# Kernel tuning notes

Measured on AMD Instinct MI355X. Metric: run time of the kernel, lower is better.

The kernel has to match this reference:

```python
import jax, jax.numpy as jnp
import numpy as np

D = 64        # state dim (num_output)
H = 256       # MLP hidden width
B = 4096      # batch
NUM_STEPS = 16  # fixed-step Dormand-Prince steps over t in [0,1] per bijector


def _mlp(t, y, W1, b1, W2, b2, W3, b3):
    # time-conditioned MLP: concat scalar t to state, two tanh layers, linear out
    tcol = jnp.full((y.shape[0], 1), t, dtype=y.dtype)
    h = jnp.tanh(jnp.concatenate([y, tcol], axis=1) @ W1 + b1)
    h = jnp.tanh(h @ W2 + b2)
    return h @ W3 + b3


def _dopri5_fixed(f, y0):
    # classic Dormand-Prince (RK45) Butcher tableau, 5th-order solution,
    # fixed step h = 1/NUM_STEPS from t=0 to t=1
    h = jnp.asarray(1.0 / NUM_STEPS, dtype=y0.dtype)

    def step(y, i):
        t = i.astype(y0.dtype) * h
        k1 = f(t, y)
        k2 = f(t + h * (1/5),  y + h * ((1/5) * k1))
        k3 = f(t + h * (3/10), y + h * ((3/40) * k1 + (9/40) * k2))
        k4 = f(t + h * (4/5),  y + h * ((44/45) * k1 - (56/15) * k2 + (32/9) * k3))
        k5 = f(t + h * (8/9),  y + h * ((19372/6561) * k1 - (25360/2187) * k2
                                        + (64448/6561) * k3 - (212/729) * k4))
        k6 = f(t + h,          y + h * ((9017/3168) * k1 - (355/33) * k2
                                        + (46732/5247) * k3 + (49/176) * k4
                                        - (5103/18656) * k5))
        y_next = y + h * ((35/384) * k1 + (500/1113) * k3 + (125/192) * k4
                          - (2187/6784) * k5 + (11/84) * k6)
        return y_next, None

    y_final, _ = jax.lax.scan(step, y0, jnp.arange(NUM_STEPS))
    return y_final


def setup_inputs() -> dict:
    key = jax.random.key(0)
    ks = jax.random.split(key, 7)
    s_in = 1.0 / np.sqrt(D + 1)
    s_h = 1.0 / np.sqrt(H)
    inp = {"x": jax.random.normal(ks[0], (B, D), dtype=jnp.float32)}
    for i, base in enumerate([1, 4]):
        inp[f"p{i}_W1"] = jax.random.normal(ks[base], (D + 1, H), dtype=jnp.float32) * s_in
        inp[f"p{i}_b1"] = jnp.zeros((H,), dtype=jnp.float32)
        inp[f"p{i}_W2"] = jax.random.normal(ks[base + 1], (H, H), dtype=jnp.float32) * s_h
        inp[f"p{i}_b2"] = jnp.zeros((H,), dtype=jnp.float32)
        inp[f"p{i}_W3"] = jax.random.normal(ks[base + 2], (H, D), dtype=jnp.float32) * s_h
        inp[f"p{i}_b3"] = jnp.zeros((D,), dtype=jnp.float32)
    return inp


def reference(x, p0_W1, p0_b1, p0_W2, p0_b2, p0_W3, p0_b3,
              p1_W1, p1_b1, p1_W2, p1_b2, p1_W3, p1_b3):
    # Chain(list(reversed(bijectors))).forward applies bijector 0 first, then 1.
    # FFJORD bijector forward = integrate dz/dt = mlp(t, z) from t=0 to t=1.
    y = x
    params = [(p0_W1, p0_b1, p0_W2, p0_b2, p0_W3, p0_b3),
              (p1_W1, p1_b1, p1_W2, p1_b2, p1_W3, p1_b3)]
    for (W1, b1, W2, b2, W3, b3) in params:
        f = lambda t, z: _mlp(t, z, W1, b1, W2, b2, W3, b3)
        y = _dopri5_fixed(f, y)
    return y
```

## Files before the change

kernel.cpp:

```cpp
#include <hip/hip_runtime.h>

typedef __attribute__((ext_vector_type(8))) short short8;
typedef __attribute__((ext_vector_type(4))) float f32x4;

#define NSTEPS 16

__device__ __forceinline__ unsigned short bf16rne(float f) {
  unsigned int u = __float_as_uint(f);
  u += 0x7FFFu + ((u >> 16) & 1u);
  return (unsigned short)(u >> 16);
}

#if __has_builtin(__builtin_amdgcn_cvt_pk_bf16_f32)
typedef __attribute__((ext_vector_type(2))) __bf16 v2bf16;
__device__ __forceinline__ unsigned int pk2(float a, float b) {
  v2bf16 t = __builtin_amdgcn_cvt_pk_bf16_f32(a, b);
  unsigned int r;
  __builtin_memcpy(&r, &t, 4);
  return r;
}
#else
__device__ __forceinline__ unsigned int pk2(float a, float b) {
  unsigned int ua = __float_as_uint(a), ub = __float_as_uint(b);
  ua += 0x7FFFu + ((ua >> 16) & 1u);
  ub += 0x7FFFu + ((ub >> 16) & 1u);
  return (ua >> 16) | (ub & 0xFFFF0000u);
}
#endif

__device__ __forceinline__ float tanh_fast(float x) {
  float e = __builtin_amdgcn_exp2f(x * 2.8853900817779268f);
  return __builtin_fmaf(-2.0f, __builtin_amdgcn_rcpf(e + 1.0f), 1.0f);
}

__global__ void ffjord_setup(const float* __restrict__ W1a, const float* __restrict__ W2a,
                             const float* __restrict__ W3a, const float* __restrict__ W1b,
                             const float* __restrict__ W2b, const float* __restrict__ W3b,
                             unsigned short* __restrict__ ws) {
  int gid = blockIdx.x * blockDim.x + threadIdx.x;
  int bij = gid / 12288;
  int r = gid - bij * 12288;
  const float* W1 = bij ? W1b : W1a;
  const float* W2 = bij ? W2b : W2a;
  const float* W3 = bij ? W3b : W3a;
  unsigned short* o = ws + bij * 98304;
  const float* src;
  int kstride;
  if (r < 2048) {
    int lane = r & 63, nt = (r >> 6) & 15, ks = r >> 10;
    int k0 = ks * 32 + (lane >> 4) * 8, n = nt * 16 + (lane & 15);
    src = W1 + k0 * 256 + n; kstride = 256; o += r * 8;
  } else if (r < 10240) {
    int rr = r - 2048;
    int lane = rr & 63, nt = (rr >> 6) & 15, ks = rr >> 10;
    int k0 = ks * 32 + (lane >> 4) * 8, n = nt * 16 + (lane & 15);
    src = W2 + k0 * 256 + n; kstride = 256; o += 16384 + rr * 8;
  } else {
    int rr = r - 10240;
    int lane = rr & 63, nt = (rr >> 6) & 3, ks = rr >> 8;
    int k0 = ks * 32 + (lane >> 4) * 8, n = nt * 16 + (lane & 15);
    src = W3 + k0 * 64 + n; kstride = 64; o += 81920 + rr * 8;
  }
  #pragma unroll
  for (int j = 0; j < 8; j++) o[j] = bf16rne(src[j * kstride]);
}

__global__ __launch_bounds__(512, 2) void ffjord_main(
    const float* __restrict__ x, float* __restrict__ out,
    const unsigned short* __restrict__ ws,
    const float* __restrict__ W1a, const float* __restrict__ b1a,
    const float* __restrict__ b2a, const float* __restrict__ b3a,
    const float* __restrict__ W1b, const float* __restrict__ b1b,
    const float* __restrict__ b2b, const float* __restrict__ b3b) {
  __shared__ __align__(16) unsigned short zA[1088];
  __shared__ __align__(16) unsigned short h1A[4096];
  __shared__ __align__(16) unsigned short h2A[4096];
  __shared__ __align__(16) float fbuf[2][16 * 68];

  const int tid = threadIdx.x;
  const int wave = tid >> 6;
  const int lane = tid & 63;
  const int cl = lane & 15;
  const int qd = lane >> 4;
  const int kh = wave >> 2;
  const int mt3 = wave & 3;
  const int c3 = mt3 * 16 + qd * 4;
  const int row0 = blockIdx.x * 16;
  const int row = tid >> 5;
  const int d0 = (tid & 31) * 2;

  const int zoff = ((d0 >> 5) * 4 + ((d0 >> 3) & 3)) * 136 + row * 8 + (d0 & 7);
  const int zrb = qd * 136 + cl * 8;

  int hoff[2];
  #pragma unroll
  for (int t = 0; t < 2; t++) {
    int c0 = (wave * 2 + t) * 16 + qd * 4;
    hoff[t] = (c0 >> 5) * 512 + ((c0 & 31) >> 3) * 128 + cl * 8 + (c0 & 7);
  }

  const float hstep = 1.0f / 16.0f;

  float y[2];
  {
    float2 v = *(const float2*)(x + (row0 + row) * 64 + d0);
    y[0] = v.x; y[1] = v.y;
  }
  float k[6][2];

  const float ACO[6][5] = {
      {0.f, 0.f, 0.f, 0.f, 0.f},
      {1.f / 5.f, 0.f, 0.f, 0.f, 0.f},
      {3.f / 40.f, 9.f / 40.f, 0.f, 0.f, 0.f},
      {44.f / 45.f, -56.f / 15.f, 32.f / 9.f, 0.f, 0.f},
      {19372.f / 6561.f, -25360.f / 2187.f, 64448.f / 6561.f, -212.f / 729.f, 0.f},
      {9017.f / 3168.f, -355.f / 33.f, 46732.f / 5247.f, 49.f / 176.f, -5103.f / 18656.f}};
  const float CT[6] = {0.0f, 0.2f, 0.3f, 0.8f, 8.0f / 9.0f, 1.0f};
  const float BW0 = 35.f / 384.f, BW2 = 500.f / 1113.f, BW3 = 125.f / 192.f,
              BW4 = -2187.f / 6784.f, BW5 = 11.f / 84.f;

  for (int bij = 0; bij < 2; bij++) {
    const unsigned short* wsb = ws + bij * 98304;
    const float* W1 = bij ? W1b : W1a;
    const float* b1 = bij ? b1b : b1a;
    const float* b2 = bij ? b2b : b2a;
    const float* b3 = bij ? b3b : b3a;

    f32x4 b1c[2], w1t4[2], b2c[2];
    #pragma unroll
    for (int t = 0; t < 2; t++) {
      int c0 = (wave * 2 + t) * 16 + qd * 4;
      b1c[t] = *(const f32x4*)(b1 + c0);
      w1t4[t] = *(const f32x4*)(W1 + 64 * 256 + c0);
      b2c[t] = *(const f32x4*)(b2 + c0);
    }
    f32x4 b3c;
    if (kh == 0) b3c = *(const f32x4*)(b3 + c3);
    else { b3c[0] = 0.f; b3c[1] = 0.f; b3c[2] = 0.f; b3c[3] = 0.f; }

    const short8* w1p = (const short8*)wsb;
    const short8* w2p = (const short8*)(wsb + 16384);
    const short8* w3p = (const short8*)(wsb + 81920);
    short8 w1f[2][2];
    #pragma unroll
    for (int ks = 0; ks < 2; ks++)
      #pragma unroll
      for (int t = 0; t < 2; t++)
        w1f[ks][t] = w1p[(ks * 16 + wave * 2 + t) * 64 + lane];
    short8 w2f[8][2];
    #pragma unroll
    for (int ks = 0; ks < 8; ks++)
      #pragma unroll
      for (int t = 0; t < 2; t++)
        w2f[ks][t] = w2p[(ks * 16 + wave * 2 + t) * 64 + lane];
    short8 w3f[4];
    #pragma unroll
    for (int kk = 0; kk < 4; kk++)
      w3f[kk] = w3p[((kh * 4 + kk) * 4 + mt3) * 64 + lane];

    for (int step = 0; step < NSTEPS; step++) {
      float stepf = (float)step;
      #pragma unroll
      for (int s = 0; s < 6; s++) {
        float ts = (stepf + CT[s]) * hstep;

        {
          float z0 = y[0], z1 = y[1];
          #pragma unroll
          for (int j = 0; j < 5; j++)
            if (j < s) {
              float a = hstep * ACO[s][j];
              z0 += a * k[j][0];
              z1 += a * k[j][1];
            }
          *(unsigned int*)(zA + zoff) = pk2(z0, z1);
        }
        __syncthreads();

        {
          short8 a0 = *(const short8*)(zA + zrb);
          short8 a1 = *(const short8*)(zA + zrb + 544);
          #pragma unroll
          for (int t = 0; t < 2; t++) {
            f32x4 acc;
            #pragma unroll
            for (int r = 0; r < 4; r++)
              acc[r] = __builtin_fmaf(ts, w1t4[t][r], b1c[t][r]);
            acc = __builtin_amdgcn_mfma_f32_16x16x32_bf16(w1f[0][t], a0, acc, 0, 0, 0);
            acc = __builtin_amdgcn_mfma_f32_16x16x32_bf16(w1f[1][t], a1, acc, 0, 0, 0);
            uint2 pv;
            pv.x = pk2(tanh_fast(acc[0]), tanh_fast(acc[1]));
            pv.y = pk2(tanh_fast(acc[2]), tanh_fast(acc[3]));
            *(uint2*)(h1A + hoff[t]) = pv;
          }
        }
        __syncthreads();

        {
          f32x4 accA[2], accB[2];
          #pragma unroll
          for (int t = 0; t < 2; t++) {
            accA[t] = b2c[t];
            accB[t][0] = 0.f; accB[t][1] = 0.f; accB[t][2] = 0.f; accB[t][3] = 0.f;
          }
          #pragma unroll
          for (int ks = 0; ks < 4; ks++) {
            short8 hb = ((const short8*)h1A)[ks * 64 + lane];
            accA[0] = __builtin_amdgcn_mfma_f32_16x16x32_bf16(w2f[ks][0], hb, accA[0], 0, 0, 0);
            accA[1] = __builtin_amdgcn_mfma_f32_16x16x32_bf16(w2f[ks][1], hb, accA[1], 0, 0, 0);
          }
          #pragma unroll
          for (int ks = 4; ks < 8; ks++) {
            short8 hb = ((const short8*)h1A)[ks * 64 + lane];
            accB[0] = __builtin_amdgcn_mfma_f32_16x16x32_bf16(w2f[ks][0], hb, accB[0], 0, 0, 0);
            accB[1] = __builtin_amdgcn_mfma_f32_16x16x32_bf16(w2f[ks][1], hb, accB[1], 0, 0, 0);
          }
          #pragma unroll
          for (int t = 0; t < 2; t++) {
            uint2 pv;
            pv.x = pk2(tanh_fast(accA[t][0] + accB[t][0]), tanh_fast(accA[t][1] + accB[t][1]));
            pv.y = pk2(tanh_fast(accA[t][2] + accB[t][2]), tanh_fast(accA[t][3] + accB[t][3]));
            *(uint2*)(h2A + hoff[t]) = pv;
          }
        }
        __syncthreads();

        {
          f32x4 accP = b3c;
          f32x4 accQ; accQ[0] = 0.f; accQ[1] = 0.f; accQ[2] = 0.f; accQ[3] = 0.f;
          short8 hb0 = ((const short8*)h2A)[(kh * 4 + 0) * 64 + lane];
          short8 hb1 = ((const short8*)h2A)[(kh * 4 + 1) * 64 + lane];
          short8 hb2 = ((const short8*)h2A)[(kh * 4 + 2) * 64 + lane];
          short8 hb3 = ((const short8*)h2A)[(kh * 4 + 3) * 64 + lane];
          accP = __builtin_amdgcn_mfma_f32_16x16x32_bf16(w3f[0], hb0, accP, 0, 0, 0);
          accP = __builtin_amdgcn_mfma_f32_16x16x32_bf16(w3f[1], hb1, accP, 0, 0, 0);
          accQ = __builtin_amdgcn_mfma_f32_16x16x32_bf16(w3f[2], hb2, accQ, 0, 0, 0);
          accQ = __builtin_amdgcn_mfma_f32_16x16x32_bf16(w3f[3], hb3, accQ, 0, 0, 0);
          f32x4 res;
          #pragma unroll
          for (int r = 0; r < 4; r++) res[r] = accP[r] + accQ[r];
          *(f32x4*)(&fbuf[kh][cl * 68 + c3]) = res;
        }
        __syncthreads();

        {
          float2 fa = *(const float2*)(&fbuf[0][row * 68 + d0]);
          float2 fb = *(const float2*)(&fbuf[1][row * 68 + d0]);
          k[s][0] = fa.x + fb.x;
          k[s][1] = fa.y + fb.y;
        }
      }

      #pragma unroll
      for (int i = 0; i < 2; i++) {
        float d = BW0 * k[0][i] + BW2 * k[2][i] + BW3 * k[3][i] +
                  BW4 * k[4][i] + BW5 * k[5][i];
        y[i] += hstep * d;
      }
    }
  }

  float2 o2; o2.x = y[0]; o2.y = y[1];
  *(float2*)(out + (row0 + row) * 64 + d0) = o2;
}

extern "C" void kernel_launch(void* const* d_in, const int* in_sizes, int n_in,
                              void* d_out, int out_size, void* d_ws, size_t ws_size,
                              hipStream_t stream) {
  (void)in_sizes; (void)n_in; (void)out_size; (void)ws_size;
  const float* x   = (const float*)d_in[0];
  const float* W1a = (const float*)d_in[1];
  const float* b1a = (const float*)d_in[2];
  const float* W2a = (const float*)d_in[3];
  const float* b2a = (const float*)d_in[4];
  const float* W3a = (const float*)d_in[5];
  const float* b3a = (const float*)d_in[6];
  const float* W1b = (const float*)d_in[7];
  const float* b1b = (const float*)d_in[8];
  const float* W2b = (const float*)d_in[9];
  const float* b2b = (const float*)d_in[10];
  const float* W3b = (const float*)d_in[11];
  const float* b3b = (const float*)d_in[12];
  unsigned short* ws = (unsigned short*)d_ws;
  float* out = (float*)d_out;

  hipLaunchKernelGGL(ffjord_setup, dim3(96), dim3(256), 0, stream,
                     W1a, W2a, W3a, W1b, W2b, W3b, ws);
  hipLaunchKernelGGL(ffjord_main, dim3(256), dim3(512), 0, stream,
                     x, out, ws, W1a, b1a, b2a, b3a, W1b, b1b, b2b, b3b);
}
```

Measured before the change: 332.2 us.

## Double block to 1024 threads, one 16-column tile per wave

Each block now runs 16 waves instead of 8. Every wave owns a single 16-column tile of the hidden layers instead of two, the final layer's K dimension is split four ways across waves, and each thread tracks one state element instead of two. The aim is more parallel waves per 16-row tile to hide MFMA and barrier latency in this serial RK chain, with lower register pressure per thread. In exchange there is a wider block-level __syncthreads, a four-way fbuf reduction, narrower per-thread stores, and weight fragments duplicated across more waves.

```diff
diff --git a/kernel.cpp b/kernel.cpp
--- a/kernel.cpp
+++ b/kernel.cpp
@@ -65,7 +65,7 @@
   for (int j = 0; j < 8; j++) o[j] = bf16rne(src[j * kstride]);
 }
 
-__global__ __launch_bounds__(512, 2) void ffjord_main(
+__global__ __launch_bounds__(1024, 4) void ffjord_main(
     const float* __restrict__ x, float* __restrict__ out,
     const unsigned short* __restrict__ ws,
     const float* __restrict__ W1a, const float* __restrict__ b1a,
@@ -75,38 +75,29 @@
   __shared__ __align__(16) unsigned short zA[1088];
   __shared__ __align__(16) unsigned short h1A[4096];
   __shared__ __align__(16) unsigned short h2A[4096];
-  __shared__ __align__(16) float fbuf[2][16 * 68];
+  __shared__ __align__(16) float fbuf[4][16 * 68];
 
   const int tid = threadIdx.x;
   const int wave = tid >> 6;
   const int lane = tid & 63;
   const int cl = lane & 15;
   const int qd = lane >> 4;
-  const int kh = wave >> 2;
   const int mt3 = wave & 3;
+  const int kq = wave >> 2;
   const int c3 = mt3 * 16 + qd * 4;
   const int row0 = blockIdx.x * 16;
-  const int row = tid >> 5;
-  const int d0 = (tid & 31) * 2;
+  const int row = wave;
+  const int d0 = lane;
 
   const int zoff = ((d0 >> 5) * 4 + ((d0 >> 3) & 3)) * 136 + row * 8 + (d0 & 7);
   const int zrb = qd * 136 + cl * 8;
-
-  int hoff[2];
-  #pragma unroll
-  for (int t = 0; t < 2; t++) {
-    int c0 = (wave * 2 + t) * 16 + qd * 4;
-    hoff[t] = (c0 >> 5) * 512 + ((c0 & 31) >> 3) * 128 + cl * 8 + (c0 & 7);
-  }
+  const int c0 = wave * 16 + qd * 4;
+  const int hoff = (c0 >> 5) * 512 + ((c0 & 31) >> 3) * 128 + cl * 8 + (c0 & 7);
 
   const float hstep = 1.0f / 16.0f;
 
-  float y[2];
-  {
-    float2 v = *(const float2*)(x + (row0 + row) * 64 + d0);
-    y[0] = v.x; y[1] = v.y;
-  }
-  float k[6][2];
+  float y = x[(row0 + row) * 64 + d0];
+  float k[6];
 
   const float ACO[6][5] = {
       {0.f, 0.f, 0.f, 0.f, 0.f},
@@ -126,37 +117,28 @@
     const float* b2 = bij ? b2b : b2a;
     const float* b3 = bij ? b3b : b3a;
 
-    f32x4 b1c[2], w1t4[2], b2c[2];
-    #pragma unroll
-    for (int t = 0; t < 2; t++) {
-      int c0 = (wave * 2 + t) * 16 + qd * 4;
-      b1c[t] = *(const f32x4*)(b1 + c0);
-      w1t4[t] = *(const f32x4*)(W1 + 64 * 256 + c0);
-      b2c[t] = *(const f32x4*)(b2 + c0);
-    }
+    f32x4 b1c = *(const f32x4*)(b1 + c0);
+    f32x4 w1t4 = *(const f32x4*)(W1 + 64 * 256 + c0);
+    f32x4 b2c = *(const f32x4*)(b2 + c0);
     f32x4 b3c;
-    if (kh == 0) b3c = *(const f32x4*)(b3 + c3);
+    if (kq == 0) b3c = *(const f32x4*)(b3 + c3);
     else { b3c[0] = 0.f; b3c[1] = 0.f; b3c[2] = 0.f; b3c[3] = 0.f; }
 
     const short8* w1p = (const short8*)wsb;
     const short8* w2p = (const short8*)(wsb + 16384);
     const short8* w3p = (const short8*)(wsb + 81920);
-    short8 w1f[2][2];
+    short8 w1f[2];
     #pragma unroll
     for (int ks = 0; ks < 2; ks++)
-      #pragma unroll
-      for (int t = 0; t < 2; t++)
-        w1f[ks][t] = w1p[(ks * 16 + wave * 2 + t) * 64 + lane];
-    short8 w2f[8][2];
+      w1f[ks] = w1p[(ks * 16 + wave) * 64 + lane];
+    short8 w2f[8];
     #pragma unroll
     for (int ks = 0; ks < 8; ks++)
-      #pragma unroll
-      for (int t = 0; t < 2; t++)
-        w2f[ks][t] = w2p[(ks * 16 + wave * 2 + t) * 64 + lane];
-    short8 w3f[4];
+      w2f[ks] = w2p[(ks * 16 + wave) * 64 + lane];
+    short8 w3f[2];
     #pragma unroll
-    for (int kk = 0; kk < 4; kk++)
-      w3f[kk] = w3p[((kh * 4 + kk) * 4 + mt3) * 64 + lane];
+    for (int kk = 0; kk < 2; kk++)
+      w3f[kk] = w3p[((kq * 2 + kk) * 4 + mt3) * 64 + lane];
 
     for (int step = 0; step < NSTEPS; step++) {
       float stepf = (float)step;
@@ -165,103 +147,71 @@
         float ts = (stepf + CT[s]) * hstep;
 
         {
-          float z0 = y[0], z1 = y[1];
+          float z = y;
           #pragma unroll
           for (int j = 0; j < 5; j++)
-            if (j < s) {
-              float a = hstep * ACO[s][j];
-              z0 += a * k[j][0];
-              z1 += a * k[j][1];
-            }
-          *(unsigned int*)(zA + zoff) = pk2(z0, z1);
+            if (j < s) z += (hstep * ACO[s][j]) * k[j];
+          zA[zoff] = bf16rne(z);
         }
         __syncthreads();
 
         {
           short8 a0 = *(const short8*)(zA + zrb);
           short8 a1 = *(const short8*)(zA + zrb + 544);
-          #pragma unroll
-          for (int t = 0; t < 2; t++) {
-            f32x4 acc;
-            #pragma unroll
-            for (int r = 0; r < 4; r++)
-              acc[r] = __builtin_fmaf(ts, w1t4[t][r], b1c[t][r]);
-            acc = __builtin_amdgcn_mfma_f32_16x16x32_bf16(w1f[0][t], a0, acc, 0, 0, 0);
-            acc = __builtin_amdgcn_mfma_f32_16x16x32_bf16(w1f[1][t], a1, acc, 0, 0, 0);
-            uint2 pv;
-            pv.x = pk2(tanh_fast(acc[0]), tanh_fast(acc[1]));
-            pv.y = pk2(tanh_fast(acc[2]), tanh_fast(acc[3]));
-            *(uint2*)(h1A + hoff[t]) = pv;
-          }
-        }
-        __syncthreads();
-
-        {
-          f32x4 accA[2], accB[2];
-          #pragma unroll
-          for (int t = 0; t < 2; t++) {
-            accA[t] = b2c[t];
-            accB[t][0] = 0.f; accB[t][1] = 0.f; accB[t][2] = 0.f; accB[t][3] = 0.f;
-          }
+          f32x4 acc;
+          #pragma unroll
+          for (int r = 0; r < 4; r++)
+            acc[r] = __builtin_fmaf(ts, w1t4[r], b1c[r]);
+          acc = __builtin_amdgcn_mfma_f32_16x16x32_bf16(w1f[0], a0, acc, 0, 0, 0);
+          acc = __builtin_amdgcn_mfma_f32_16x16x32_bf16(w1f[1], a1, acc, 0, 0, 0);
+          uint2 pv;
+          pv.x = pk2(tanh_fast(acc[0]), tanh_fast(acc[1]));
+          pv.y = pk2(tanh_fast(acc[2]), tanh_fast(acc[3]));
+          *(uint2*)(h1A + hoff) = pv;
+        }
+        __syncthreads();
+
+        {
+          f32x4 accA = b2c;
+          f32x4 accB; accB[0] = 0.f; accB[1] = 0.f; accB[2] = 0.f; accB[3] = 0.f;
           #pragma unroll
           for (int ks = 0; ks < 4; ks++) {
             short8 hb = ((const short8*)h1A)[ks * 64 + lane];
-            accA[0] = __builtin_amdgcn_mfma_f32_16x16x32_bf16(w2f[ks][0], hb, accA[0], 0, 0, 0);
-            accA[1] = __builtin_amdgcn_mfma_f32_16x16x32_bf16(w2f[ks][1], hb, accA[1], 0, 0, 0);
+            accA = __builtin_amdgcn_mfma_f32_16x16x32_bf16(w2f[ks], hb, accA, 0, 0, 0);
           }
           #pragma unroll
           for (int ks = 4; ks < 8; ks++) {
             short8 hb = ((const short8*)h1A)[ks * 64 + lane];
-            accB[0] = __builtin_amdgcn_mfma_f32_16x16x32_bf16(w2f[ks][0], hb, accB[0], 0, 0, 0);
-            accB[1] = __builtin_amdgcn_mfma_f32_16x16x32_bf16(w2f[ks][1], hb, accB[1], 0, 0, 0);
+            accB = __builtin_amdgcn_mfma_f32_16x16x32_bf16(w2f[ks], hb, accB, 0, 0, 0);
           }
-          #pragma unroll
-          for (int t = 0; t < 2; t++) {
-            uint2 pv;
-            pv.x = pk2(tanh_fast(accA[t][0] + accB[t][0]), tanh_fast(accA[t][1] + accB[t][1]));
-            pv.y = pk2(tanh_fast(accA[t][2] + accB[t][2]), tanh_fast(accA[t][3] + accB[t][3]));
-            *(uint2*)(h2A + hoff[t]) = pv;
-          }
-        }
-        __syncthreads();
-
-        {
+          uint2 pv;
+          pv.x = pk2(tanh_fast(accA[0] + accB[0]), tanh_fast(accA[1] + accB[1]));
+          pv.y = pk2(tanh_fast(accA[2] + accB[2]), tanh_fast(accA[3] + accB[3]));
+          *(uint2*)(h2A + hoff) = pv;
+        }
+        __syncthreads();
+
+        {
+          short8 hb0 = ((const short8*)h2A)[(kq * 2 + 0) * 64 + lane];
+          short8 hb1 = ((const short8*)h2A)[(kq * 2 + 1) * 64 + lane];
           f32x4 accP = b3c;
-          f32x4 accQ; accQ[0] = 0.f; accQ[1] = 0.f; accQ[2] = 0.f; accQ[3] = 0.f;
-          short8 hb0 = ((const short8*)h2A)[(kh * 4 + 0) * 64 + lane];
-          short8 hb1 = ((const short8*)h2A)[(kh * 4 + 1) * 64 + lane];
-          short8 hb2 = ((const short8*)h2A)[(kh * 4 + 2) * 64 + lane];
-          short8 hb3 = ((const short8*)h2A)[(kh * 4 + 3) * 64 + lane];
           accP = __builtin_amdgcn_mfma_f32_16x16x32_bf16(w3f[0], hb0, accP, 0, 0, 0);
           accP = __builtin_amdgcn_mfma_f32_16x16x32_bf16(w3f[1], hb1, accP, 0, 0, 0);
-          accQ = __builtin_amdgcn_mfma_f32_16x16x32_bf16(w3f[2], hb2, accQ, 0, 0, 0);
-          accQ = __builtin_amdgcn_mfma_f32_16x16x32_bf16(w3f[3], hb3, accQ, 0, 0, 0);
-          f32x4 res;
-          #pragma unroll
-          for (int r = 0; r < 4; r++) res[r] = accP[r] + accQ[r];
-          *(f32x4*)(&fbuf[kh][cl * 68 + c3]) = res;
-        }
-        __syncthreads();
-
-        {
-          float2 fa = *(const float2*)(&fbuf[0][row * 68 + d0]);
-          float2 fb = *(const float2*)(&fbuf[1][row * 68 + d0]);
-          k[s][0] = fa.x + fb.x;
-          k[s][1] = fa.y + fb.y;
+          *(f32x4*)(&fbuf[kq][cl * 68 + c3]) = accP;
+        }
+        __syncthreads();
+
+        {
+          int fo = row * 68 + d0;
+          k[s] = (fbuf[0][fo] + fbuf[1][fo]) + (fbuf[2][fo] + fbuf[3][fo]);
         }
       }
 
-      #pragma unroll
-      for (int i = 0; i < 2; i++) {
-        float d = BW0 * k[0][i] + BW2 * k[2][i] + BW3 * k[3][i] +
-                  BW4 * k[4][i] + BW5 * k[5][i];
-        y[i] += hstep * d;
-      }
+      y += hstep * (BW0 * k[0] + BW2 * k[2] + BW3 * k[3] + BW4 * k[4] + BW5 * k[5]);
     }
   }
 
-  float2 o2; o2.x = y[0]; o2.y = y[1];
-  *(float2*)(out + (row0 + row) * 64 + d0) = o2;
+  out[(row0 + row) * 64 + d0] = y;
 }
 
 extern "C" void kernel_launch(void* const* d_in, const int* in_sizes, int n_in,
@@ -286,6 +236,6 @@
 
   hipLaunchKernelGGL(ffjord_setup, dim3(96), dim3(256), 0, stream,
                      W1a, W2a, W3a, W1b, W2b, W3b, ws);
-  hipLaunchKernelGGL(ffjord_main, dim3(256), dim3(512), 0, stream,
+  hipLaunchKernelGGL(ffjord_main, dim3(256), dim3(1024), 0, stream,
                      x, out, ws, W1a, b1a, b2a, b3a, W1b, b1b, b2b, b3b);
 }
```

Result: no change. 327.1 us (-1.5%).
